# Kernel tuning notes

Measured on AMD Instinct MI355X. Metric: run time of the kernel, lower is better.

Reference implementation:

```python
import jax, jax.numpy as jnp
import numpy as np

B, SQ, SE = 16, 1024, 1024
C_IN, C_ENC, DK, DV, H = 256, 256, 64, 64, 8
BN_EPS = 1e-5
NEG_SLOPE = 0.01  # torch LeakyReLU default


def setup_inputs() -> dict:
    key = jax.random.key(0)
    ks = jax.random.split(key, 8)
    x = jax.random.normal(ks[0], (B, SE, C_ENC), dtype=jnp.float32)
    q = jax.random.normal(ks[1], (B, SQ, C_IN), dtype=jnp.float32)
    # per-head 1x1-conv projection weights, stacked over heads
    Wq = jax.random.normal(ks[2], (H, DK, C_IN), dtype=jnp.float32) / np.sqrt(C_IN)
    Wk = jax.random.normal(ks[3], (H, DK, C_ENC), dtype=jnp.float32) / np.sqrt(C_ENC)
    Wv = jax.random.normal(ks[4], (H, DV, C_ENC), dtype=jnp.float32) / np.sqrt(C_ENC)
    # output projection (Conv1d(H*DV -> C_IN, k=1, bias=False))
    Wp = jax.random.normal(ks[5], (C_IN, H * DV), dtype=jnp.float32) / np.sqrt(H * DV)
    gamma = jax.random.normal(ks[6], (C_IN,), dtype=jnp.float32) * 0.1 + 1.0
    beta = jax.random.normal(ks[7], (C_IN,), dtype=jnp.float32) * 0.1
    return {"x": x, "q": q, "Wq": Wq, "Wk": Wk, "Wv": Wv, "Wp": Wp,
            "gamma": gamma, "beta": beta}


def reference(x, q, Wq, Wk, Wv, Wp, gamma, beta):
    # per-head Q/K/V via 1x1 conv == einsum over channel dim
    qh = jnp.einsum('bsc,hdc->bhsd', q, Wq)   # [B,H,SQ,DK]
    kh = jnp.einsum('btc,hdc->bhtd', x, Wk)   # [B,H,SE,DK]
    vh = jnp.einsum('btc,hec->bhte', x, Wv)   # [B,H,SE,DV]
    scale = 1.0 / jnp.sqrt(jnp.asarray(DK, dtype=qh.dtype))
    scores = jnp.einsum('bhsd,bhtd->bhst', qh, kh) * scale  # [B,H,SQ,SE]
    attn = jax.nn.softmax(scores, axis=-1)
    oh = jnp.einsum('bhst,bhte->bhse', attn, vh)  # [B,H,SQ,DV]
    # concat heads along feature dim (head-major order, as torch.cat over dim=2)
    o = jnp.transpose(oh, (0, 2, 1, 3)).reshape(B, SQ, H * DV)
    # LBRD projection: 1x1 conv -> BatchNorm1d (train mode: batch stats) -> LeakyReLU
    p = jnp.einsum('bsf,cf->bsc', o, Wp)  # [B,SQ,C_IN]
    mean = jnp.mean(p, axis=(0, 1))        # per-channel over (B, L)
    var = jnp.var(p, axis=(0, 1))          # biased, matching torch BN normalization
    y = (p - mean) * jax.lax.rsqrt(var + BN_EPS) * gamma + beta
    return jnp.where(y >= 0, y, NEG_SLOPE * y)
```

## Files before the change

### kernel.cpp

```cpp
#include <hip/hip_runtime.h>
#include <cstddef>

#define B_    16
#define SQ_   1024
#define SE_   1024
#define CIN_  256
#define DK_   64
#define H_    8
#define HD_   512
#define NROWS 16384
#define BN_EPS 1e-5f
#define NEG_SLOPE 0.01f

typedef __attribute__((ext_vector_type(8))) short bf16x8;
typedef __attribute__((ext_vector_type(4))) float f32x4;

#define BAR()        __builtin_amdgcn_s_barrier()
#define WAIT_LGKM0() asm volatile("s_waitcnt lgkmcnt(0)" ::: "memory")

__device__ __forceinline__ unsigned short f2bf(float f) {
    unsigned int u = __float_as_uint(f);
    return (unsigned short)((u + 0x7FFFu + ((u >> 16) & 1u)) >> 16);
}

#if __has_builtin(__builtin_amdgcn_perm)
__device__ __forceinline__ unsigned int pack_trunc(float lo, float hi) {
    return __builtin_amdgcn_perm(__float_as_uint(hi), __float_as_uint(lo), 0x07060302u);
}
#else
__device__ __forceinline__ unsigned int pack_trunc(float lo, float hi) {
    return (__float_as_uint(lo) >> 16) | (__float_as_uint(hi) & 0xFFFF0000u);
}
#endif

#if __has_builtin(__builtin_amdgcn_exp2f)
#define EXP2F(x) __builtin_amdgcn_exp2f(x)
#else
#define EXP2F(x) exp2f(x)
#endif

__device__ __forceinline__ ushort4 pack4(f32x4 v) {
    ushort4 p;
    p.x = f2bf(v[0]); p.y = f2bf(v[1]);
    p.z = f2bf(v[2]); p.w = f2bf(v[3]);
    return p;
}

__device__ __forceinline__ bf16x8 cvt8(float4 f0, float4 f1) {
    uint4 pk;
    pk.x = pack_trunc(f0.x, f0.y);
    pk.y = pack_trunc(f0.z, f0.w);
    pk.z = pack_trunc(f1.x, f1.y);
    pk.w = pack_trunc(f1.z, f1.w);
    return *(bf16x8*)&pk;
}

__global__ __launch_bounds__(256) void wcast(const float* __restrict__ Wq,
                                             const float* __restrict__ Wk,
                                             const float* __restrict__ Wv,
                                             const float* __restrict__ Wp,
                                             unsigned short* __restrict__ dWq,
                                             unsigned short* __restrict__ dWkv,
                                             unsigned short* __restrict__ dWp,
                                             float* __restrict__ stats) {
    if (blockIdx.x < 2) stats[blockIdx.x * 256 + threadIdx.x] = 0.f;
    int i = blockIdx.x * 256 + threadIdx.x;
    int which = i >> 15, off = i & 32767;
    const float* s; unsigned short* d; float sc = 1.0f;
    if (which == 0)      { s = Wq; d = dWq; sc = 0.18033688011112042f; }
    else if (which == 1) { s = Wk; d = dWkv; }
    else if (which == 2) { s = Wv; d = dWkv + 131072; }
    else                 { s = Wp; d = dWp; }
    float4 v = *(const float4*)(s + (size_t)off * 4);
    ushort4 pk;
    pk.x = f2bf(v.x * sc); pk.y = f2bf(v.y * sc);
    pk.z = f2bf(v.z * sc); pk.w = f2bf(v.w * sc);
    *(ushort4*)(d + (size_t)off * 4) = pk;
}

__global__ __launch_bounds__(256) void gemm_qkv9(const float* __restrict__ qsrc,
                                                 const float* __restrict__ xsrc,
                                                 const unsigned short* __restrict__ Wqb,
                                                 const unsigned short* __restrict__ Wkvb,
                                                 unsigned short* __restrict__ qh,
                                                 unsigned short* __restrict__ khb,
                                                 unsigned short* __restrict__ vTb) {
    __shared__ __align__(16) unsigned short smem[32768];
    unsigned short* Ws = smem;
    unsigned short* Cs = smem;

    const int tid = threadIdx.x;
    const int w = tid >> 6, l = tid & 63, lq = l >> 4, lr = l & 15;

    const int flat = blockIdx.x;
    const int xcd  = flat & 7;
    const int jj   = flat >> 3;
    const int bx   = jj % 12;
    const int by   = (jj / 12) + xcd * 16;

    const bool isQ = bx < 4;
    const bool isV = bx >= 8;
    const float* A = isQ ? qsrc : xsrc;
    const unsigned short* W = isQ ? Wqb : Wkvb;
    const int n0 = (isQ ? bx : bx - 4) * 128;
    const int m0 = by * 128;

    f32x4 acc[2][8] = {};
    float4 aA[8], aB[8];

    const float* A0 = A + (size_t)(m0 + w * 32 + lr) * 256 + lq * 8;
    const float* A1 = A + (size_t)(m0 + w * 32 + 16 + lr) * 256 + lq * 8;

#define LOAD_A(buf, kstep) do {                                              \
        buf[0] = *(const float4*)(A0 + (kstep) * 64);                        \
        buf[1] = *(const float4*)(A0 + (kstep) * 64 + 4);                    \
        buf[2] = *(const float4*)(A0 + (kstep) * 64 + 32);                   \
        buf[3] = *(const float4*)(A0 + (kstep) * 64 + 36);                   \
        buf[4] = *(const float4*)(A1 + (kstep) * 64);                        \
        buf[5] = *(const float4*)(A1 + (kstep) * 64 + 4);                    \
        buf[6] = *(const float4*)(A1 + (kstep) * 64 + 32);                   \
        buf[7] = *(const float4*)(A1 + (kstep) * 64 + 36);                   \
    } while (0)

#define QKV_STEP(buf, kstep) do {                                            \
        _Pragma("unroll")                                                    \
        for (int ks = 0; ks < 2; ++ks) {                                     \
            bf16x8 a0 = cvt8(buf[ks * 2], buf[ks * 2 + 1]);                  \
            bf16x8 a1 = cvt8(buf[4 + ks * 2], buf[4 + ks * 2 + 1]);          \
            const int colu = (kstep) * 8 + ks * 4 + lq;                      \
            const int cswz = colu ^ (lr & 7);                                \
            if (!isV) {                                                      \
                _Pragma("unroll")                                            \
                for (int j = 0; j < 8; ++j) {                                \
                    bf16x8 bb = *(bf16x8*)&Ws[((j * 16 + lr) * 32 + cswz) * 8]; \
                    acc[0][j] = __builtin_amdgcn_mfma_f32_16x16x32_bf16(bb, a0, acc[0][j], 0, 0, 0); \
                    acc[1][j] = __builtin_amdgcn_mfma_f32_16x16x32_bf16(bb, a1, acc[1][j], 0, 0, 0); \
                }                                                            \
            } else {                                                         \
                _Pragma("unroll")                                            \
                for (int j = 0; j < 8; ++j) {                                \
                    bf16x8 bb = *(bf16x8*)&Ws[((j * 16 + lr) * 32 + cswz) * 8]; \
                    acc[0][j] = __builtin_amdgcn_mfma_f32_16x16x32_bf16(a0, bb, acc[0][j], 0, 0, 0); \
                    acc[1][j] = __builtin_amdgcn_mfma_f32_16x16x32_bf16(a1, bb, acc[1][j], 0, 0, 0); \
                }                                                            \
            }                                                                \
        }                                                                    \
    } while (0)

    LOAD_A(aA, 0);

    #pragma unroll
    for (int i = 0; i < 16; ++i) {
        int u = tid + i * 256;
        int row = u >> 5, colu = u & 31;
        uint4 v = *(const uint4*)(W + (size_t)(n0 + row) * 256 + colu * 8);
        *(uint4*)&Ws[(row * 32 + (colu ^ (row & 7))) * 8] = v;
    }
    __syncthreads();

    LOAD_A(aB, 1);
    QKV_STEP(aA, 0);
    LOAD_A(aA, 2);
    QKV_STEP(aB, 1);
    LOAD_A(aB, 3);
    QKV_STEP(aA, 2);
    QKV_STEP(aB, 3);

#undef LOAD_A
#undef QKV_STEP

    __syncthreads();
    const int c16 = tid & 15;
    const int rb  = tid >> 4;
    if (!isV) {
        #pragma unroll
        for (int mf = 0; mf < 2; ++mf)
            #pragma unroll
            for (int j = 0; j < 8; ++j)
                *(ushort4*)&Cs[(w * 32 + mf * 16 + lr) * 144 + j * 16 + lq * 4] =
                    pack4(acc[mf][j]);
        __syncthreads();
        unsigned short* C = isQ ? qh : khb;
        #pragma unroll
        for (int it = 0; it < 8; ++it) {
            int r = it * 16 + rb;
            *(uint4*)(C + (size_t)(m0 + r) * 512 + n0 + c16 * 8) =
                *(const uint4*)(Cs + r * 144 + c16 * 8);
        }
    } else {
        #pragma unroll
        for (int mf = 0; mf < 2; ++mf)
            #pragma unroll
            for (int j = 0; j < 8; ++j)
                *(ushort4*)&Cs[(j * 16 + lr) * 144 + w * 32 + mf * 16 + lq * 4] =
                    pack4(acc[mf][j]);
        __syncthreads();
        const int bb = m0 >> 10, t0 = m0 & 1023;
        #pragma unroll
        for (int it = 0; it < 8; ++it) {
            int el = it * 16 + rb;
            int colv = n0 - 512 + el;
            int hh = colv >> 6, e = colv & 63;
            *(uint4*)(vTb + (size_t)((bb * 8 + hh) * 64 + e) * 1024 + t0 + c16 * 8) =
                *(const uint4*)(Cs + el * 144 + c16 * 8);
        }
    }
}

__global__ __launch_bounds__(256) void attn_mfma12(const unsigned short* __restrict__ qh,
                                                   const unsigned short* __restrict__ kh,
                                                   const unsigned short* __restrict__ vT,
                                                   unsigned short* __restrict__ o) {
    __shared__ __align__(16) unsigned short Ks[64 * 64];
    __shared__ __align__(16) unsigned short Vs[64 * 64];
    __shared__ __align__(16) unsigned short Ps[4][64 * 40];

    const int tid = threadIdx.x;
    const int w = tid >> 6, l = tid & 63, lq = l >> 4, lr = l & 15;

    const int flat = blockIdx.x;
    const int xcd  = flat & 7;
    const int jj   = flat >> 3;
    const int q0   = (jj & 3) * 256;
    const int hb   = (jj >> 2) + xcd * 16;
    const int h    = hb & 7;
    const int b    = hb >> 3;

    const int swz = (lr & 7) << 3;

    bf16x8 qf[4][2];
    #pragma unroll
    for (int mm = 0; mm < 4; ++mm) {
        const unsigned short* qr =
            qh + (size_t)(b * SQ_ + q0 + w * 64 + mm * 16 + lr) * HD_ + h * DK_;
        qf[mm][0] = *(const bf16x8*)(qr + lq * 8);
        qf[mm][1] = *(const bf16x8*)(qr + 32 + lq * 8);
    }

    const unsigned short* kb = kh + (size_t)(b * SE_) * HD_ + h * DK_;
    const unsigned short* vb = vT + (size_t)((b * 8 + h) * 64) * 1024;

    const int se = tid >> 3;
    const int sc = (tid & 7) * 8;
    const int sswz = (se & 7) << 3;

    float l_i[4] = {};
    f32x4 oacc[4][4] = {};
    unsigned short* Pw = Ps[w];

    uint4 kR[2], vR[2];
    #pragma unroll
    for (int ps = 0; ps < 2; ++ps) {
        int rr = se + ps * 32;
        kR[ps] = *(const uint4*)(kb + (size_t)rr * HD_ + sc);
        vR[ps] = *(const uint4*)(vb + (size_t)rr * 1024 + sc);
    }

    for (int t0 = 0; t0 < SE_; t0 += 64) {
        BAR();
        #pragma unroll
        for (int ps = 0; ps < 2; ++ps) {
            int rr = se + ps * 32;
            int ad = ((rr * 64 + sc) ^ sswz);
            *(uint4*)&Ks[ad] = kR[ps];
            *(uint4*)&Vs[ad] = vR[ps];
        }
        if (t0 + 64 < SE_) {
            #pragma unroll
            for (int ps = 0; ps < 2; ++ps) {
                int rr = se + ps * 32;
                kR[ps] = *(const uint4*)(kb + (size_t)(t0 + 64 + rr) * HD_ + sc);
                vR[ps] = *(const uint4*)(vb + (size_t)rr * 1024 + t0 + 64 + sc);
            }
        }
        WAIT_LGKM0();
        BAR();

        f32x4 s0[2][4] = {};
        __builtin_amdgcn_s_setprio(1);
        #pragma unroll
        for (int ks = 0; ks < 2; ++ks)
            #pragma unroll
            for (int tt = 0; tt < 2; ++tt) {
                bf16x8 kf = *(bf16x8*)&Ks[((tt * 16 + lr) * 64 + ks * 32 + lq * 8) ^ swz];
                #pragma unroll
                for (int mm = 0; mm < 4; ++mm)
                    s0[tt][mm] = __builtin_amdgcn_mfma_f32_16x16x32_bf16(kf, qf[mm][ks], s0[tt][mm], 0, 0, 0);
            }
        __builtin_amdgcn_s_setprio(0);

        #pragma unroll
        for (int mm = 0; mm < 4; ++mm)
            #pragma unroll
            for (int tt = 0; tt < 2; ++tt) {
                float e0 = EXP2F(s0[tt][mm][0]);
                float e1 = EXP2F(s0[tt][mm][1]);
                float e2 = EXP2F(s0[tt][mm][2]);
                float e3 = EXP2F(s0[tt][mm][3]);
                l_i[mm] += (e0 + e1) + (e2 + e3);
                uint2 pk;
                pk.x = pack_trunc(e0, e1);
                pk.y = pack_trunc(e2, e3);
                *(uint2*)&Pw[(mm * 16 + lr) * 40 + tt * 16 + lq * 4] = pk;
            }

        f32x4 s1[2][4] = {};
        __builtin_amdgcn_s_setprio(1);
        #pragma unroll
        for (int ks = 0; ks < 2; ++ks)
            #pragma unroll
            for (int tt = 0; tt < 2; ++tt) {
                bf16x8 kf = *(bf16x8*)&Ks[(((tt + 2) * 16 + lr) * 64 + ks * 32 + lq * 8) ^ swz];
                #pragma unroll
                for (int mm = 0; mm < 4; ++mm)
                    s1[tt][mm] = __builtin_amdgcn_mfma_f32_16x16x32_bf16(kf, qf[mm][ks], s1[tt][mm], 0, 0, 0);
            }
        __builtin_amdgcn_s_setprio(0);

        asm volatile("s_waitcnt lgkmcnt(0)" ::: "memory");

        __builtin_amdgcn_s_setprio(1);
        {
            bf16x8 pf[4];
            #pragma unroll
            for (int mm = 0; mm < 4; ++mm)
                pf[mm] = *(bf16x8*)&Pw[(mm * 16 + lr) * 40 + lq * 8];
            #pragma unroll
            for (int j = 0; j < 4; ++j) {
                bf16x8 vf = *(bf16x8*)&Vs[((j * 16 + lr) * 64 + lq * 8) ^ swz];
                #pragma unroll
                for (int mm = 0; mm < 4; ++mm)
                    oacc[mm][j] = __builtin_amdgcn_mfma_f32_16x16x32_bf16(vf, pf[mm], oacc[mm][j], 0, 0, 0);
            }
        }
        __builtin_amdgcn_s_setprio(0);

        #pragma unroll
        for (int mm = 0; mm < 4; ++mm)
            #pragma unroll
            for (int tt = 0; tt < 2; ++tt) {
                float e0 = EXP2F(s1[tt][mm][0]);
                float e1 = EXP2F(s1[tt][mm][1]);
                float e2 = EXP2F(s1[tt][mm][2]);
                float e3 = EXP2F(s1[tt][mm][3]);
                l_i[mm] += (e0 + e1) + (e2 + e3);
                uint2 pk;
                pk.x = pack_trunc(e0, e1);
                pk.y = pack_trunc(e2, e3);
                *(uint2*)&Pw[(mm * 16 + lr) * 40 + tt * 16 + lq * 4] = pk;
            }

        asm volatile("s_waitcnt lgkmcnt(0)" ::: "memory");

        __builtin_amdgcn_s_setprio(1);
        {
            bf16x8 pf[4];
            #pragma unroll
            for (int mm = 0; mm < 4; ++mm)
                pf[mm] = *(bf16x8*)&Pw[(mm * 16 + lr) * 40 + lq * 8];
            #pragma unroll
            for (int j = 0; j < 4; ++j) {
                bf16x8 vf = *(bf16x8*)&Vs[((j * 16 + lr) * 64 + 32 + lq * 8) ^ swz];
                #pragma unroll
                for (int mm = 0; mm < 4; ++mm)
                    oacc[mm][j] = __builtin_amdgcn_mfma_f32_16x16x32_bf16(vf, pf[mm], oacc[mm][j], 0, 0, 0);
            }
        }
        __builtin_amdgcn_s_setprio(0);
    }

    float inv[4];
    #pragma unroll
    for (int mm = 0; mm < 4; ++mm) {
        float t = l_i[mm];
        t += __shfl_xor(t, 16);
        t += __shfl_xor(t, 32);
        inv[mm] = 1.0f / t;
    }

    #pragma unroll
    for (int mm = 0; mm < 4; ++mm)
        #pragma unroll
        for (int j = 0; j < 4; ++j) {
            f32x4 v = oacc[mm][j];
            v[0] *= inv[mm]; v[1] *= inv[mm]; v[2] *= inv[mm]; v[3] *= inv[mm];
            *(ushort4*)&o[(size_t)(b * SQ_ + q0 + w * 64 + mm * 16 + lr) * HD_ +
                          h * DK_ + j * 16 + lq * 4] = pack4(v);
        }
}

__global__ __launch_bounds__(256) void gemm_out3(const unsigned short* __restrict__ A,
                                                 const unsigned short* __restrict__ W,
                                                 float* __restrict__ C,
                                                 float* __restrict__ gsum,
                                                 float* __restrict__ gsumsq) {
    __shared__ __align__(16) unsigned short Ws[32768];
    const int tid = threadIdx.x;
    const int w = tid >> 6, l = tid & 63, lq = l >> 4, lr = l & 15;
    const int n0 = blockIdx.x * 64, m0 = blockIdx.y * 128;
    const int K = 512;

    f32x4 acc[2][4] = {};
    uint4 aA[4], aB[4];

    const unsigned short* A0 = A + (size_t)(m0 + w * 32 + lr) * K + lq * 8;
    const unsigned short* A1 = A + (size_t)(m0 + w * 32 + 16 + lr) * K + lq * 8;

#define LOADO(buf, kstep) do {                                               \
        buf[0] = *(const uint4*)(A0 + (kstep) * 64);                         \
        buf[1] = *(const uint4*)(A0 + (kstep) * 64 + 32);                    \
        buf[2] = *(const uint4*)(A1 + (kstep) * 64);                         \
        buf[3] = *(const uint4*)(A1 + (kstep) * 64 + 32);                    \
    } while (0)

#define OSTEP(buf, kstep) do {                                               \
        _Pragma("unroll")                                                    \
        for (int ks = 0; ks < 2; ++ks) {                                     \
            bf16x8 a0 = *(bf16x8*)&buf[ks];                                  \
            bf16x8 a1 = *(bf16x8*)&buf[2 + ks];                              \
            const int cu = (kstep) * 8 + ks * 4 + lq;                        \
            const int cswz = cu ^ (lr & 7);                                  \
            _Pragma("unroll")                                                \
            for (int j = 0; j < 4; ++j) {                                    \
                bf16x8 bb = *(bf16x8*)&Ws[((j * 16 + lr) * 64 + cswz) * 8];  \
                acc[0][j] = __builtin_amdgcn_mfma_f32_16x16x32_bf16(a0, bb, acc[0][j], 0, 0, 0); \
                acc[1][j] = __builtin_amdgcn_mfma_f32_16x16x32_bf16(a1, bb, acc[1][j], 0, 0, 0); \
            }                                                                \
        }                                                                    \
    } while (0)

    LOADO(aA, 0);

    #pragma unroll
    for (int i = 0; i < 16; ++i) {
        int u = tid + i * 256;
        int row = u >> 6, cu = u & 63;
        uint4 v = *(const uint4*)(W + (size_t)(n0 + row) * 512 + cu * 8);
        *(uint4*)&Ws[(row * 64 + (cu ^ (row & 7))) * 8] = v;
    }
    __syncthreads();

    LOADO(aB, 1); OSTEP(aA, 0);
    LOADO(aA, 2); OSTEP(aB, 1);
    LOADO(aB, 3); OSTEP(aA, 2);
    LOADO(aA, 4); OSTEP(aB, 3);
    LOADO(aB, 5); OSTEP(aA, 4);
    LOADO(aA, 6); OSTEP(aB, 5);
    LOADO(aB, 7); OSTEP(aA, 6);
    OSTEP(aB, 7);

#undef LOADO
#undef OSTEP

    float cs[4] = {}, cq[4] = {};
    #pragma unroll
    for (int m = 0; m < 2; ++m)
        #pragma unroll
        for (int j = 0; j < 4; ++j)
            #pragma unroll
            for (int r = 0; r < 4; ++r) {
                float v = acc[m][j][r];
                C[(size_t)(m0 + w * 32 + m * 16 + lq * 4 + r) * 256 + n0 + j * 16 + lr] = v;
                cs[j] += v;
                cq[j] += v * v;
            }
    #pragma unroll
    for (int j = 0; j < 4; ++j) {
        cs[j] += __shfl_xor(cs[j], 16); cs[j] += __shfl_xor(cs[j], 32);
        cq[j] += __shfl_xor(cq[j], 16); cq[j] += __shfl_xor(cq[j], 32);
    }
    __syncthreads();
    float* red = (float*)Ws;
    if (lq == 0) {
        #pragma unroll
        for (int j = 0; j < 4; ++j) {
            red[w * 128 + j * 16 + lr]      = cs[j];
            red[w * 128 + 64 + j * 16 + lr] = cq[j];
        }
    }
    __syncthreads();
    if (tid < 128) {
        int col = tid & 63, stat = tid >> 6;
        float t = red[stat * 64 + col] + red[128 + stat * 64 + col] +
                  red[256 + stat * 64 + col] + red[384 + stat * 64 + col];
        atomicAdd((stat ? gsumsq : gsum) + n0 + col, t);
    }
}

__global__ __launch_bounds__(256) void bn_norm4(const float* __restrict__ p,
                                                const float* __restrict__ gsum,
                                                const float* __restrict__ gsumsq,
                                                const float* __restrict__ gamma,
                                                const float* __restrict__ beta,
                                                float* __restrict__ out) {
    int i = blockIdx.x * 256 + threadIdx.x;
    int c0 = (i * 4) & 255;
    const float invN = 1.0f / (float)NROWS;
    float4 pv = *(const float4*)(p + (size_t)i * 4);
    float vals[4] = {pv.x, pv.y, pv.z, pv.w};
    float res[4];
    #pragma unroll
    for (int k = 0; k < 4; ++k) {
        int c = c0 + k;
        float mean = gsum[c] * invN;
        float var  = gsumsq[c] * invN - mean * mean;
        float v = (vals[k] - mean) * rsqrtf(var + BN_EPS) * gamma[c] + beta[c];
        res[k] = v >= 0.f ? v : NEG_SLOPE * v;
    }
    float4 ov = {res[0], res[1], res[2], res[3]};
    *(float4*)(out + (size_t)i * 4) = ov;
}

extern "C" void kernel_launch(void* const* d_in, const int* in_sizes, int n_in,
                              void* d_out, int out_size, void* d_ws, size_t ws_size,
                              hipStream_t stream) {
    const float* x     = (const float*)d_in[0];
    const float* q     = (const float*)d_in[1];
    const float* Wq    = (const float*)d_in[2];
    const float* Wk    = (const float*)d_in[3];
    const float* Wv    = (const float*)d_in[4];
    const float* Wp    = (const float*)d_in[5];
    const float* gamma = (const float*)d_in[6];
    const float* beta  = (const float*)d_in[7];
    float* out = (float*)d_out;

    char* base = (char*)d_ws;
    unsigned short* Wqb  = (unsigned short*)(base + 0);
    unsigned short* Wkvb = (unsigned short*)(base + 262144);
    unsigned short* Wpb  = (unsigned short*)(base + 786432);
    unsigned short* qh   = (unsigned short*)(base + 1048576);
    unsigned short* khb  = (unsigned short*)(base + 17825792);
    unsigned short* vTb  = (unsigned short*)(base + 34603008);
    unsigned short* ob   = (unsigned short*)(base + 51380224);
    float*          pbuf = (float*)        (base + 68157440);
    float*          stats= (float*)        (base + 84934656);

    wcast<<<512, 256, 0, stream>>>(Wq, Wk, Wv, Wp, Wqb, Wkvb, Wpb, stats);

    gemm_qkv9<<<1536, 256, 0, stream>>>(q, x, Wqb, Wkvb, qh, khb, vTb);

    attn_mfma12<<<512, 256, 0, stream>>>(qh, khb, vTb, ob);

    gemm_out3<<<dim3(4, 128), 256, 0, stream>>>(ob, Wpb, pbuf, stats, stats + 256);

    bn_norm4<<<4096, 256, 0, stream>>>(pbuf, stats, stats + 256, gamma, beta, out);
}
```

Measured before the change: 201.6 us.

## Split attention key sequence across two warp groups and merge partial outputs

The attention kernel now uses 512 threads per block, split into two groups of four waves. Each group processes half of the key/value sequence with its own K/V/P shared-memory tiles. The partial output accumulators and row sums are then combined through shared memory before normalization and store. This doubles the waves working on each query tile to raise parallelism and latency hiding on 512 blocks. The cost is a shared-memory reduction, a larger LDS footprint and fewer resident blocks per CU.

```diff
diff --git a/kernel.cpp b/kernel.cpp
--- a/kernel.cpp
+++ b/kernel.cpp
@@ -207,16 +207,17 @@
     }
 }
 
-__global__ __launch_bounds__(256) void attn_mfma12(const unsigned short* __restrict__ qh,
+__global__ __launch_bounds__(512) void attn_mfma15(const unsigned short* __restrict__ qh,
                                                    const unsigned short* __restrict__ kh,
                                                    const unsigned short* __restrict__ vT,
                                                    unsigned short* __restrict__ o) {
-    __shared__ __align__(16) unsigned short Ks[64 * 64];
-    __shared__ __align__(16) unsigned short Vs[64 * 64];
-    __shared__ __align__(16) unsigned short Ps[4][64 * 40];
+    __shared__ __align__(16) unsigned short smem[36864];
 
     const int tid = threadIdx.x;
-    const int w = tid >> 6, l = tid & 63, lq = l >> 4, lr = l & 15;
+    const int w8 = tid >> 6;
+    const int grp = w8 >> 2;
+    const int w = w8 & 3;
+    const int l = tid & 63, lq = l >> 4, lr = l & 15;
 
     const int flat = blockIdx.x;
     const int xcd  = flat & 7;
@@ -228,6 +229,10 @@
 
     const int swz = (lr & 7) << 3;
 
+    unsigned short* Kg = smem + grp * 4096;
+    unsigned short* Vg = smem + 8192 + grp * 4096;
+    unsigned short* Pw = smem + 16384 + w8 * 2560;
+
     bf16x8 qf[4][2];
     #pragma unroll
     for (int mm = 0; mm < 4; ++mm) {
@@ -237,16 +242,16 @@
         qf[mm][1] = *(const bf16x8*)(qr + 32 + lq * 8);
     }
 
-    const unsigned short* kb = kh + (size_t)(b * SE_) * HD_ + h * DK_;
-    const unsigned short* vb = vT + (size_t)((b * 8 + h) * 64) * 1024;
-
-    const int se = tid >> 3;
-    const int sc = (tid & 7) * 8;
+    const unsigned short* kb = kh + (size_t)(b * SE_ + grp * 512) * HD_ + h * DK_;
+    const unsigned short* vb = vT + (size_t)((b * 8 + h) * 64) * 1024 + grp * 512;
+
+    const int gtid = tid & 255;
+    const int se = gtid >> 3;
+    const int sc = (gtid & 7) * 8;
     const int sswz = (se & 7) << 3;
 
     float l_i[4] = {};
     f32x4 oacc[4][4] = {};
-    unsigned short* Pw = Ps[w];
 
     uint4 kR[2], vR[2];
     #pragma unroll
@@ -256,16 +261,16 @@
         vR[ps] = *(const uint4*)(vb + (size_t)rr * 1024 + sc);
     }
 
-    for (int t0 = 0; t0 < SE_; t0 += 64) {
+    for (int t0 = 0; t0 < 512; t0 += 64) {
         BAR();
         #pragma unroll
         for (int ps = 0; ps < 2; ++ps) {
             int rr = se + ps * 32;
             int ad = ((rr * 64 + sc) ^ sswz);
-            *(uint4*)&Ks[ad] = kR[ps];
-            *(uint4*)&Vs[ad] = vR[ps];
-        }
-        if (t0 + 64 < SE_) {
+            *(uint4*)&Kg[ad] = kR[ps];
+            *(uint4*)&Vg[ad] = vR[ps];
+        }
+        if (t0 + 64 < 512) {
             #pragma unroll
             for (int ps = 0; ps < 2; ++ps) {
                 int rr = se + ps * 32;
@@ -282,7 +287,7 @@
         for (int ks = 0; ks < 2; ++ks)
             #pragma unroll
             for (int tt = 0; tt < 2; ++tt) {
-                bf16x8 kf = *(bf16x8*)&Ks[((tt * 16 + lr) * 64 + ks * 32 + lq * 8) ^ swz];
+                bf16x8 kf = *(bf16x8*)&Kg[((tt * 16 + lr) * 64 + ks * 32 + lq * 8) ^ swz];
                 #pragma unroll
                 for (int mm = 0; mm < 4; ++mm)
                     s0[tt][mm] = __builtin_amdgcn_mfma_f32_16x16x32_bf16(kf, qf[mm][ks], s0[tt][mm], 0, 0, 0);
@@ -310,7 +315,7 @@
         for (int ks = 0; ks < 2; ++ks)
             #pragma unroll
             for (int tt = 0; tt < 2; ++tt) {
-                bf16x8 kf = *(bf16x8*)&Ks[(((tt + 2) * 16 + lr) * 64 + ks * 32 + lq * 8) ^ swz];
+                bf16x8 kf = *(bf16x8*)&Kg[(((tt + 2) * 16 + lr) * 64 + ks * 32 + lq * 8) ^ swz];
                 #pragma unroll
                 for (int mm = 0; mm < 4; ++mm)
                     s1[tt][mm] = __builtin_amdgcn_mfma_f32_16x16x32_bf16(kf, qf[mm][ks], s1[tt][mm], 0, 0, 0);
@@ -327,7 +332,7 @@
                 pf[mm] = *(bf16x8*)&Pw[(mm * 16 + lr) * 40 + lq * 8];
             #pragma unroll
             for (int j = 0; j < 4; ++j) {
-                bf16x8 vf = *(bf16x8*)&Vs[((j * 16 + lr) * 64 + lq * 8) ^ swz];
+                bf16x8 vf = *(bf16x8*)&Vg[((j * 16 + lr) * 64 + lq * 8) ^ swz];
                 #pragma unroll
                 for (int mm = 0; mm < 4; ++mm)
                     oacc[mm][j] = __builtin_amdgcn_mfma_f32_16x16x32_bf16(vf, pf[mm], oacc[mm][j], 0, 0, 0);
@@ -360,7 +365,7 @@
                 pf[mm] = *(bf16x8*)&Pw[(mm * 16 + lr) * 40 + lq * 8];
             #pragma unroll
             for (int j = 0; j < 4; ++j) {
-                bf16x8 vf = *(bf16x8*)&Vs[((j * 16 + lr) * 64 + 32 + lq * 8) ^ swz];
+                bf16x8 vf = *(bf16x8*)&Vg[((j * 16 + lr) * 64 + 32 + lq * 8) ^ swz];
                 #pragma unroll
                 for (int mm = 0; mm < 4; ++mm)
                     oacc[mm][j] = __builtin_amdgcn_mfma_f32_16x16x32_bf16(vf, pf[mm], oacc[mm][j], 0, 0, 0);
@@ -369,24 +374,52 @@
         __builtin_amdgcn_s_setprio(0);
     }
 
-    float inv[4];
-    #pragma unroll
-    for (int mm = 0; mm < 4; ++mm) {
-        float t = l_i[mm];
-        t += __shfl_xor(t, 16);
-        t += __shfl_xor(t, 32);
-        inv[mm] = 1.0f / t;
-    }
-
-    #pragma unroll
-    for (int mm = 0; mm < 4; ++mm)
-        #pragma unroll
-        for (int j = 0; j < 4; ++j) {
-            f32x4 v = oacc[mm][j];
-            v[0] *= inv[mm]; v[1] *= inv[mm]; v[2] *= inv[mm]; v[3] *= inv[mm];
-            *(ushort4*)&o[(size_t)(b * SQ_ + q0 + w * 64 + mm * 16 + lr) * HD_ +
-                          h * DK_ + j * 16 + lq * 4] = pack4(v);
-        }
+    __syncthreads();
+    float* ms = (float*)smem;
+    if (grp == 1) {
+        #pragma unroll
+        for (int mm = 0; mm < 4; ++mm)
+            #pragma unroll
+            for (int j = 0; j < 4; ++j)
+                *(f32x4*)&ms[(w * 16 + mm * 4 + j) * 256 + l * 4] = oacc[mm][j];
+        #pragma unroll
+        for (int mm = 0; mm < 4; ++mm) {
+            float t = l_i[mm];
+            t += __shfl_xor(t, 16);
+            t += __shfl_xor(t, 32);
+            if (lq == 0) ms[16384 + w * 64 + mm * 16 + lr] = t;
+        }
+    }
+    __syncthreads();
+    if (grp == 0) {
+        float inv[4];
+        #pragma unroll
+        for (int mm = 0; mm < 4; ++mm) {
+            #pragma unroll
+            for (int j = 0; j < 4; ++j) {
+                f32x4 other = *(const f32x4*)&ms[(w * 16 + mm * 4 + j) * 256 + l * 4];
+                oacc[mm][j][0] += other[0];
+                oacc[mm][j][1] += other[1];
+                oacc[mm][j][2] += other[2];
+                oacc[mm][j][3] += other[3];
+            }
+            float t = l_i[mm];
+            t += __shfl_xor(t, 16);
+            t += __shfl_xor(t, 32);
+            t += ms[16384 + w * 64 + mm * 16 + lr];
+            inv[mm] = 1.0f / t;
+        }
+
+        #pragma unroll
+        for (int mm = 0; mm < 4; ++mm)
+            #pragma unroll
+            for (int j = 0; j < 4; ++j) {
+                f32x4 v = oacc[mm][j];
+                v[0] *= inv[mm]; v[1] *= inv[mm]; v[2] *= inv[mm]; v[3] *= inv[mm];
+                *(ushort4*)&o[(size_t)(b * SQ_ + q0 + w * 64 + mm * 16 + lr) * HD_ +
+                              h * DK_ + j * 16 + lq * 4] = pack4(v);
+            }
+    }
 }
 
 __global__ __launch_bounds__(256) void gemm_out3(const unsigned short* __restrict__ A,
@@ -539,7 +572,7 @@
 
     gemm_qkv9<<<1536, 256, 0, stream>>>(q, x, Wqb, Wkvb, qh, khb, vTb);
 
-    attn_mfma12<<<512, 256, 0, stream>>>(qh, khb, vTb, ob);
+    attn_mfma15<<<512, 512, 0, stream>>>(qh, khb, vTb, ob);
 
     gemm_out3<<<dim3(4, 128), 256, 0, stream>>>(ob, Wpb, pbuf, stats, stats + 256);
 
```

Measured after the change: 218.6 us. 1.08x slower.
